# Performance work log

Hardware: AMD Instinct MI355X
Metric: run time of the kernel (lower is better)

Reference implementation:

```python
import jax, jax.numpy as jnp
import numpy as np

B, S, H, I, E = 2, 2048, 1024, 2048, 8
TOP_K = 2

def setup_inputs() -> dict:
    key = jax.random.key(0)
    k1, k2, k3, k4 = jax.random.split(key, 4)
    hidden_states = jax.random.normal(k1, (B, S, H), dtype=jnp.float32)
    # gate initialized xavier_uniform with gain=0.1 -> small weights
    gate_w = jax.random.normal(k2, (E, H), dtype=jnp.float32) * 0.02
    w_up = jax.random.normal(k3, (E, H, I), dtype=jnp.float32) * 0.02
    w_down = jax.random.normal(k4, (E, I, H), dtype=jnp.float32) * 0.02
    return {"hidden_states": hidden_states, "gate_w": gate_w, "w_up": w_up, "w_down": w_down}

def reference(hidden_states, gate_w, w_up, w_down):
    b, s, h = hidden_states.shape
    e = gate_w.shape[0]
    x = hidden_states.reshape(-1, h)            # [T, H]
    T = x.shape[0]

    # --- Router (eval mode: no jitter noise) ---
    logits = x @ gate_w.T                       # [T, E]
    probs = jax.nn.softmax(logits, axis=-1)
    weights, idx = jax.lax.top_k(probs, TOP_K)  # [T, K]
    weights = weights / (weights.sum(axis=-1, keepdims=True) + 1e-9)

    # Combine weights as a [T, E] scatter of the normalized top-k probs
    combine = jnp.zeros((T, e), dtype=x.dtype)
    combine = combine.at[jnp.arange(T)[:, None], idx].add(weights)

    # --- Expert FFN (silu), computed for all experts then weighted-combined ---
    hmid = jax.nn.silu(jnp.einsum('th,ehi->tei', x, w_up))   # [T, E, I]
    y = jnp.einsum('tei,eih->teh', hmid, w_down)             # [T, E, H]
    out = jnp.einsum('te,teh->th', combine, y)               # [T, H]
    return out.reshape(b, s, h)
```

## Files before the change

kernel.cpp:

```cpp
#include <hip/hip_runtime.h>
#include <math.h>

#define T_TOK 4096
#define H_DIM 1024
#define I_DIM 2048
#define E_NUM 8
#define CAP   2048
#define BM 128
#define BN 128
#define BK 64

typedef __attribute__((ext_vector_type(8))) short bf16x8;
typedef __attribute__((ext_vector_type(4))) float f32x4;

__device__ __forceinline__ unsigned short f2bf(float f) {
    union { float f; unsigned int u; } v; v.f = f;
    unsigned int r = v.u + 0x7FFFu + ((v.u >> 16) & 1u);
    return (unsigned short)(r >> 16);
}

__device__ __forceinline__ void gl_lds16(const void* g, void* l) {
    __builtin_amdgcn_global_load_lds(
        (const __attribute__((address_space(1))) void*)g,
        (__attribute__((address_space(3))) void*)l, 16, 0, 0);
}

__global__ __launch_bounds__(256) void moe_router(
    const float* __restrict__ x, const float* __restrict__ gate,
    int* __restrict__ topk_idx, float* __restrict__ topk_w)
{
    const int wave = threadIdx.x >> 6;
    const int lane = threadIdx.x & 63;
    const int t = blockIdx.x * 4 + wave;

    float acc[E_NUM];
#pragma unroll
    for (int e = 0; e < E_NUM; ++e) acc[e] = 0.f;
    const float* xp = x + (size_t)t * H_DIM;
    for (int k = lane; k < H_DIM; k += 64) {
        const float xv = xp[k];
#pragma unroll
        for (int e = 0; e < E_NUM; ++e) acc[e] += xv * gate[e * H_DIM + k];
    }
#pragma unroll
    for (int e = 0; e < E_NUM; ++e) {
#pragma unroll
        for (int off = 32; off > 0; off >>= 1)
            acc[e] += __shfl_xor(acc[e], off, 64);
    }
    if (lane == 0) {
        float m = acc[0];
#pragma unroll
        for (int e = 1; e < E_NUM; ++e) m = fmaxf(m, acc[e]);
        float p[E_NUM]; float Z = 0.f;
#pragma unroll
        for (int e = 0; e < E_NUM; ++e) { p[e] = expf(acc[e] - m); Z += p[e]; }
        const float invZ = 1.f / Z;
        int i1 = 0, i2 = 0; float v1 = -1.f, v2 = -1.f;
#pragma unroll
        for (int e = 0; e < E_NUM; ++e) {
            const float pe = p[e] * invZ;
            if (pe > v1)      { v2 = v1; i2 = i1; v1 = pe; i1 = e; }
            else if (pe > v2) { v2 = pe; i2 = e; }
        }
        const float s = 1.f / (v1 + v2 + 1e-9f);
        topk_idx[t * 2 + 0] = i1; topk_idx[t * 2 + 1] = i2;
        topk_w[t * 2 + 0] = v1 * s; topk_w[t * 2 + 1] = v2 * s;
    }
}

__global__ void moe_build(
    const int* __restrict__ topk_idx, const float* __restrict__ topk_w,
    int* __restrict__ counts, int* __restrict__ list_tok, float* __restrict__ list_w)
{
    const int t = blockIdx.x * blockDim.x + threadIdx.x;
    if (t >= T_TOK) return;
#pragma unroll
    for (int k = 0; k < 2; ++k) {
        const int e = topk_idx[t * 2 + k];
        const float w = topk_w[t * 2 + k];
        const int pos = atomicAdd(&counts[e], 1);
        if (pos < CAP) {
            list_tok[e * CAP + pos] = t;
            list_w[e * CAP + pos] = w;
        }
    }
}

__global__ __launch_bounds__(256) void moe_gather(
    const float* __restrict__ x, const int* __restrict__ counts,
    const int* __restrict__ list_tok, unsigned short* __restrict__ Xg)
{
    const int e = blockIdx.y;
    const int r = blockIdx.x;
    if (r >= min(counts[e], CAP)) return;
    const int tok = list_tok[e * CAP + r];
    const float4 v = ((const float4*)(x + (size_t)tok * H_DIM))[threadIdx.x];
    ushort4 o = make_ushort4(f2bf(v.x), f2bf(v.y), f2bf(v.z), f2bf(v.w));
    *(ushort4*)(Xg + (size_t)(e * CAP + r) * H_DIM + threadIdx.x * 4) = o;
}

__global__ __launch_bounds__(256) void transpose_bf16(
    const float* __restrict__ in, unsigned short* __restrict__ outp, int R, int C)
{
    __shared__ unsigned short t[64][72];
    const int e = blockIdx.z;
    const float* src = in + (size_t)e * R * C;
    unsigned short* dst = outp + (size_t)e * R * C;
    const int c0 = blockIdx.x * 64;
    const int r0 = blockIdx.y * 64;
    const int tx = (threadIdx.x & 15) << 2;
    const int ty = threadIdx.x >> 4;
#pragma unroll
    for (int s = 0; s < 4; ++s) {
        const int r = ty + s * 16;
        const float4 v = *(const float4*)&src[(size_t)(r0 + r) * C + c0 + tx];
        t[tx + 0][r] = f2bf(v.x);
        t[tx + 1][r] = f2bf(v.y);
        t[tx + 2][r] = f2bf(v.z);
        t[tx + 3][r] = f2bf(v.w);
    }
    __syncthreads();
    const int cc = threadIdx.x >> 3;
    const int rr = (threadIdx.x & 7) << 3;
#pragma unroll
    for (int s = 0; s < 2; ++s) {
        const int c = cc + s * 32;
        *(bf16x8*)&dst[(size_t)(c0 + c) * R + r0 + rr] = *(const bf16x8*)&t[c][rr];
    }
}

__global__ __launch_bounds__(256) void moe_gemm1(
    const unsigned short* __restrict__ Xg, const unsigned short* __restrict__ WupT,
    const int* __restrict__ counts, unsigned short* __restrict__ hmid)
{
    __shared__ unsigned short As[2][BM][BK];
    __shared__ unsigned short Bs[2][BN][BK];
    const int s_id = blockIdx.x;
    const int l = (s_id & 7) * 256 + (s_id >> 3);
    const int e = l >> 8;
    const int bx = l & 15;
    const int by = (l >> 4) & 15;
    const int cnt = min(counts[e], CAP);
    const int row0 = bx * BM;
    if (row0 >= cnt) return;
    const int n0 = by * BN;
    const int tid = threadIdx.x;
    const int lane = tid & 63;
    const int wid = tid >> 6;
    const int wm = wid >> 1, wn = wid & 1;

    const unsigned short* Ae = Xg + (size_t)e * CAP * H_DIM;
    const unsigned short* Be = WupT + (size_t)e * (size_t)I_DIM * H_DIM;

    const int sub = lane >> 3;
    const int kus = (lane & 7) * 8;

#define STAGE1(buf, kt)                                                       \
    {                                                                         \
        _Pragma("unroll")                                                     \
        for (int c = 0; c < 4; ++c) {                                         \
            const int row = (c * 4 + wid) * 8 + sub;                          \
            gl_lds16(Ae + (size_t)(row0 + row) * H_DIM + (kt) + kus,          \
                     (char*)&As[buf][0][0] + (c * 4 + wid) * 1024);           \
            gl_lds16(Be + (size_t)(n0 + row) * H_DIM + (kt) + kus,            \
                     (char*)&Bs[buf][0][0] + (c * 4 + wid) * 1024);           \
        }                                                                     \
    }

    f32x4 acc[4][4];
#pragma unroll
    for (int m = 0; m < 4; ++m)
#pragma unroll
        for (int n = 0; n < 4; ++n) acc[m][n] = (f32x4){0.f, 0.f, 0.f, 0.f};

    STAGE1(0, 0);
    __syncthreads();
    int cur = 0;
    for (int kt = 0; kt < H_DIM; kt += BK) {
        if (kt + BK < H_DIM) STAGE1(cur ^ 1, kt + BK);
#pragma unroll
        for (int kk = 0; kk < BK; kk += 32) {
            const int koff = kk + 8 * (lane >> 4);
            bf16x8 a[4], b[4];
#pragma unroll
            for (int m = 0; m < 4; ++m)
                a[m] = *(const bf16x8*)&As[cur][wm * 64 + m * 16 + (lane & 15)][koff];
#pragma unroll
            for (int n = 0; n < 4; ++n)
                b[n] = *(const bf16x8*)&Bs[cur][wn * 64 + n * 16 + (lane & 15)][koff];
#pragma unroll
            for (int m = 0; m < 4; ++m)
#pragma unroll
                for (int n = 0; n < 4; ++n)
                    acc[m][n] = __builtin_amdgcn_mfma_f32_16x16x32_bf16(
                        a[m], b[n], acc[m][n], 0, 0, 0);
        }
        __syncthreads();
        cur ^= 1;
    }
#undef STAGE1

    unsigned short* He = hmid + (size_t)e * CAP * I_DIM;
#pragma unroll
    for (int m = 0; m < 4; ++m) {
        const int rb = row0 + wm * 64 + m * 16 + ((lane >> 4) << 2);
#pragma unroll
        for (int n = 0; n < 4; ++n) {
            const int col = n0 + wn * 64 + n * 16 + (lane & 15);
#pragma unroll
            for (int j = 0; j < 4; ++j) {
                const float v = acc[m][n][j];
                const float s = v / (1.f + __expf(-v));
                He[(size_t)(rb + j) * I_DIM + col] = f2bf(s);
            }
        }
    }
}

__global__ __launch_bounds__(256) void moe_gemm2(
    const unsigned short* __restrict__ hmid, const unsigned short* __restrict__ WdownT,
    const int* __restrict__ counts, const int* __restrict__ list_tok,
    const float* __restrict__ list_w, float* __restrict__ out)
{
    __shared__ unsigned short As[2][BM][BK];
    __shared__ unsigned short Bs[2][BN][BK];
    const int s_id = blockIdx.x;
    const int l = (s_id & 7) * 256 + (s_id >> 3);
    const int e = l >> 8;
    const int bx = l & 15;
    const int by = (l >> 4) & 7;
    const int kh = (l >> 7) & 1;
    const int cnt = min(counts[e], CAP);
    const int row0 = bx * BM;
    if (row0 >= cnt) return;
    const int n0 = by * BN;
    const int kbase = kh * (I_DIM / 2);
    const int tid = threadIdx.x;
    const int lane = tid & 63;
    const int wid = tid >> 6;
    const int wm = wid >> 1, wn = wid & 1;

    const unsigned short* Ae = hmid + (size_t)e * CAP * I_DIM;
    const unsigned short* Be = WdownT + (size_t)e * (size_t)H_DIM * I_DIM;

    const int sub = lane >> 3;
    const int kus = (lane & 7) * 8;

#define STAGE2(buf, kt)                                                       \
    {                                                                         \
        _Pragma("unroll")                                                     \
        for (int c = 0; c < 4; ++c) {                                         \
            const int row = (c * 4 + wid) * 8 + sub;                          \
            gl_lds16(Ae + (size_t)(row0 + row) * I_DIM + kbase + (kt) + kus,  \
                     (char*)&As[buf][0][0] + (c * 4 + wid) * 1024);           \
            gl_lds16(Be + (size_t)(n0 + row) * I_DIM + kbase + (kt) + kus,    \
                     (char*)&Bs[buf][0][0] + (c * 4 + wid) * 1024);           \
        }                                                                     \
    }

    f32x4 acc[4][4];
#pragma unroll
    for (int m = 0; m < 4; ++m)
#pragma unroll
        for (int n = 0; n < 4; ++n) acc[m][n] = (f32x4){0.f, 0.f, 0.f, 0.f};

    STAGE2(0, 0);
    __syncthreads();
    int cur = 0;
    for (int kt = 0; kt < I_DIM / 2; kt += BK) {
        if (kt + BK < I_DIM / 2) STAGE2(cur ^ 1, kt + BK);
#pragma unroll
        for (int kk = 0; kk < BK; kk += 32) {
            const int koff = kk + 8 * (lane >> 4);
            bf16x8 a[4], b[4];
#pragma unroll
            for (int m = 0; m < 4; ++m)
                a[m] = *(const bf16x8*)&As[cur][wm * 64 + m * 16 + (lane & 15)][koff];
#pragma unroll
            for (int n = 0; n < 4; ++n)
                b[n] = *(const bf16x8*)&Bs[cur][wn * 64 + n * 16 + (lane & 15)][koff];
#pragma unroll
            for (int m = 0; m < 4; ++m)
#pragma unroll
                for (int n = 0; n < 4; ++n)
                    acc[m][n] = __builtin_amdgcn_mfma_f32_16x16x32_bf16(
                        a[m], b[n], acc[m][n], 0, 0, 0);
        }
        __syncthreads();
        cur ^= 1;
    }
#undef STAGE2

#pragma unroll
    for (int m = 0; m < 4; ++m) {
#pragma unroll
        for (int j = 0; j < 4; ++j) {
            const int gr = row0 + wm * 64 + m * 16 + ((lane >> 4) << 2) + j;
            if (gr < cnt) {
                const int tok = list_tok[e * CAP + gr];
                const float w = list_w[e * CAP + gr];
                float* op = out + (size_t)tok * H_DIM + n0 + wn * 64 + (lane & 15);
#pragma unroll
                for (int n = 0; n < 4; ++n)
                    atomicAdd(op + n * 16, w * acc[m][n][j]);
            }
        }
    }
}

extern "C" void kernel_launch(void* const* d_in, const int* in_sizes, int n_in,
                              void* d_out, int out_size, void* d_ws, size_t ws_size,
                              hipStream_t stream)
{
    const float* x      = (const float*)d_in[0];
    const float* gate   = (const float*)d_in[1];
    const float* w_up   = (const float*)d_in[2];
    const float* w_down = (const float*)d_in[3];
    float* out = (float*)d_out;

    char* ws = (char*)d_ws;
    int*   counts   = (int*)(ws);
    int*   topk_idx = (int*)(ws + 1024);
    float* topk_w   = (float*)(ws + 33792);
    int*   list_tok = (int*)(ws + 66560);
    float* list_w   = (float*)(ws + 132096);
    unsigned short* Xg     = (unsigned short*)(ws + 197632);
    unsigned short* WupT   = (unsigned short*)(ws + 197632 + 33554432ull);
    unsigned short* WdownT = (unsigned short*)(ws + 197632 + 67108864ull);
    unsigned short* hmid   = (unsigned short*)(ws + 197632 + 100663296ull);

    hipMemsetAsync(counts, 0, 1024, stream);
    hipMemsetAsync(out, 0, (size_t)out_size * sizeof(float), stream);

    moe_router<<<T_TOK / 4, 256, 0, stream>>>(x, gate, topk_idx, topk_w);
    moe_build<<<T_TOK / 256, 256, 0, stream>>>(topk_idx, topk_w, counts, list_tok, list_w);
    moe_gather<<<dim3(CAP, E_NUM), 256, 0, stream>>>(x, counts, list_tok, Xg);
    transpose_bf16<<<dim3(I_DIM / 64, H_DIM / 64, E_NUM), 256, 0, stream>>>(w_up, WupT, H_DIM, I_DIM);
    transpose_bf16<<<dim3(H_DIM / 64, I_DIM / 64, E_NUM), 256, 0, stream>>>(w_down, WdownT, I_DIM, H_DIM);
    moe_gemm1<<<2048, 256, 0, stream>>>(Xg, WupT, counts, hmid);
    moe_gemm2<<<2048, 256, 0, stream>>>(hmid, WdownT, counts, list_tok, list_w, out);
}
```

Before: 412.1 us.

## Swizzle LDS tiles in expert GEMMs and build expert lists deterministically

Both expert GEMMs now apply an XOR swizzle on the 16-byte chunk index when staging A/B tiles into LDS, with the matching read offsets, to remove bank conflicts on the MFMA fragment loads. Separately, the routing-list builder is rewritten to launch one block per expert. Each block scans all tokens with wave ballots and prefix sums, giving an ordered, atomic-free list and writing counts directly, which also removes the counts memset. The new builder serialises each expert's scan in a single block, a small cost set against sorted token order and one fewer launch.

```diff
diff --git a/kernel.cpp b/kernel.cpp
--- a/kernel.cpp
+++ b/kernel.cpp
@@ -69,22 +69,37 @@
     }
 }
 
-__global__ void moe_build(
+__global__ __launch_bounds__(256) void moe_build(
     const int* __restrict__ topk_idx, const float* __restrict__ topk_w,
     int* __restrict__ counts, int* __restrict__ list_tok, float* __restrict__ list_w)
 {
-    const int t = blockIdx.x * blockDim.x + threadIdx.x;
-    if (t >= T_TOK) return;
-#pragma unroll
-    for (int k = 0; k < 2; ++k) {
-        const int e = topk_idx[t * 2 + k];
-        const float w = topk_w[t * 2 + k];
-        const int pos = atomicAdd(&counts[e], 1);
-        if (pos < CAP) {
-            list_tok[e * CAP + pos] = t;
-            list_w[e * CAP + pos] = w;
-        }
-    }
+    const int e = blockIdx.x;
+    const int tid = threadIdx.x;
+    const int wv = tid >> 6, lane = tid & 63;
+    __shared__ int wsum[4];
+    int base = 0;
+    for (int c = 0; c < T_TOK; c += 256) {
+        const int t = c + tid;
+        const int i0 = topk_idx[t * 2 + 0];
+        const int i1 = topk_idx[t * 2 + 1];
+        const int match = (i0 == e) || (i1 == e);
+        const float w = (i0 == e) ? topk_w[t * 2 + 0] : topk_w[t * 2 + 1];
+        const unsigned long long mask = __ballot(match);
+        const int my = __popcll(mask & ((1ull << lane) - 1ull));
+        if (lane == 0) wsum[wv] = __popcll(mask);
+        __syncthreads();
+        int woff = 0;
+#pragma unroll
+        for (int i = 0; i < 4; ++i) if (i < wv) woff += wsum[i];
+        const int ctot = wsum[0] + wsum[1] + wsum[2] + wsum[3];
+        if (match) {
+            const int pos = base + woff + my;
+            if (pos < CAP) { list_tok[e * CAP + pos] = t; list_w[e * CAP + pos] = w; }
+        }
+        base += ctot;
+        __syncthreads();
+    }
+    if (tid == 0) counts[e] = min(base, CAP);
 }
 
 __global__ __launch_bounds__(256) void moe_gather(
@@ -129,6 +144,7 @@
         *(bf16x8*)&dst[(size_t)(c0 + c) * R + r0 + rr] = *(const bf16x8*)&t[c][rr];
     }
 }
+
 
 __global__ __launch_bounds__(256) void moe_gemm1(
     const unsigned short* __restrict__ Xg, const unsigned short* __restrict__ WupT,
@@ -154,7 +170,7 @@
     const unsigned short* Be = WupT + (size_t)e * (size_t)I_DIM * H_DIM;
 
     const int sub = lane >> 3;
-    const int kus = (lane & 7) * 8;
+    const int kus = ((lane & 7) ^ sub) * 8;
 
 #define STAGE1(buf, kt)                                                       \
     {                                                                         \
@@ -181,7 +197,7 @@
         if (kt + BK < H_DIM) STAGE1(cur ^ 1, kt + BK);
 #pragma unroll
         for (int kk = 0; kk < BK; kk += 32) {
-            const int koff = kk + 8 * (lane >> 4);
+            const int koff = ((((kk >> 3) | (lane >> 4)) ^ (lane & 7)) << 3);
             bf16x8 a[4], b[4];
 #pragma unroll
             for (int m = 0; m < 4; ++m)
@@ -245,7 +261,7 @@
     const unsigned short* Be = WdownT + (size_t)e * (size_t)H_DIM * I_DIM;
 
     const int sub = lane >> 3;
-    const int kus = (lane & 7) * 8;
+    const int kus = ((lane & 7) ^ sub) * 8;
 
 #define STAGE2(buf, kt)                                                       \
     {                                                                         \
@@ -272,7 +288,7 @@
         if (kt + BK < I_DIM / 2) STAGE2(cur ^ 1, kt + BK);
 #pragma unroll
         for (int kk = 0; kk < BK; kk += 32) {
-            const int koff = kk + 8 * (lane >> 4);
+            const int koff = ((((kk >> 3) | (lane >> 4)) ^ (lane & 7)) << 3);
             bf16x8 a[4], b[4];
 #pragma unroll
             for (int m = 0; m < 4; ++m)
@@ -330,11 +346,10 @@
     unsigned short* WdownT = (unsigned short*)(ws + 197632 + 67108864ull);
     unsigned short* hmid   = (unsigned short*)(ws + 197632 + 100663296ull);
 
-    hipMemsetAsync(counts, 0, 1024, stream);
     hipMemsetAsync(out, 0, (size_t)out_size * sizeof(float), stream);
 
     moe_router<<<T_TOK / 4, 256, 0, stream>>>(x, gate, topk_idx, topk_w);
-    moe_build<<<T_TOK / 256, 256, 0, stream>>>(topk_idx, topk_w, counts, list_tok, list_w);
+    moe_build<<<E_NUM, 256, 0, stream>>>(topk_idx, topk_w, counts, list_tok, list_w);
     moe_gather<<<dim3(CAP, E_NUM), 256, 0, stream>>>(x, counts, list_tok, Xg);
     transpose_bf16<<<dim3(I_DIM / 64, H_DIM / 64, E_NUM), 256, 0, stream>>>(w_up, WupT, H_DIM, I_DIM);
     transpose_bf16<<<dim3(H_DIM / 64, I_DIM / 64, E_NUM), 256, 0, stream>>>(w_down, WdownT, I_DIM, H_DIM);
```

New measurement: 369.3 us. 10.4% less time.
